# Performance work log

Hardware: AMD Instinct MI355X
Metric: run time of the kernel (lower is better)

The kernel has to match this reference:

```python
import jax, jax.numpy as jnp
import numpy as np

B, H, W, D, K = 64, 32, 32, 512, 64
EPS = 1e-12


def setup_inputs() -> dict:
    key = jax.random.key(0)
    k1, k2, k3 = jax.random.split(key, 3)
    inputs = jax.random.normal(k1, (B, H, W, D), dtype=jnp.float32)
    # 1x1 conv kernel (no bias) -> equivalent to a [D, K] matmul per pixel
    w = jax.random.normal(k2, (D, K), dtype=jnp.float32) * 0.02
    # cluster centers, stored in the original as (1,1,1,D,K); we keep [D, K]
    C = jax.random.normal(k3, (D, K), dtype=jnp.float32) * 0.02
    return {"inputs": inputs, "w": w, "C": C}


def _l2norm(v, axis=-1):
    return v / jnp.sqrt(jnp.sum(v * v, axis=axis, keepdims=True) + EPS)


def reference(inputs, w, C):
    # soft-assignment: 1x1 conv + softmax over clusters
    s = jnp.einsum('bhwd,dk->bhwk', inputs, w)          # [B,H,W,K]
    a = jax.nn.softmax(s, axis=-1)
    b, h, ww, d = inputs.shape
    k = w.shape[1]
    a2 = a.reshape(b, h * ww, k)                         # [B,N,K]
    x2 = inputs.reshape(b, h * ww, d)                    # [B,N,D]
    # VLAD reformulation: sum_n a[n,k]*(x[n,d] + C[d,k])
    #  = (a^T x)[k,d] + (sum_n a[n,k]) * C[d,k]
    # avoids materializing the [B,H,W,D,K] broadcast of the original
    vkd = jnp.einsum('bnk,bnd->bkd', a2, x2)             # [B,K,D]
    vkd = vkd + a2.sum(axis=1)[:, :, None] * C.T[None]   # [B,K,D]
    # intra-normalization over D (matches transpose->normalize in original)
    vkd = _l2norm(vkd, axis=-1)
    # transpose back to [B,D,K], flatten, global L2 normalize
    v = jnp.transpose(vkd, (0, 2, 1)).reshape(b, d * k)
    v = _l2norm(v, axis=-1)
    return v
```

## Files before the change

kernel.cpp:

```cpp
#include <hip/hip_runtime.h>

#define EPS 1e-12f
typedef __attribute__((ext_vector_type(8))) short short8;
typedef __attribute__((ext_vector_type(4))) float f32x4;

#define MFMA(a, b, c) __builtin_amdgcn_mfma_f32_16x16x32_bf16(a, b, c, 0, 0, 0)

__device__ __forceinline__ unsigned rne16(unsigned u) {
  return u + 0x7FFFu + ((u >> 16) & 1u);
}
__device__ __forceinline__ void split_pair(float f0, float f1,
                                           unsigned& hp, unsigned& lp) {
  unsigned u0 = __float_as_uint(f0), u1 = __float_as_uint(f1);
  unsigned r0 = rne16(u0), r1 = rne16(u1);
  float h0 = __uint_as_float(r0 & 0xFFFF0000u);
  float h1 = __uint_as_float(r1 & 0xFFFF0000u);
  hp = (r0 >> 16) | (r1 & 0xFFFF0000u);
  unsigned v0 = rne16(__float_as_uint(f0 - h0));
  unsigned v1 = rne16(__float_as_uint(f1 - h1));
  lp = (v0 >> 16) | (v1 & 0xFFFF0000u);
}
__device__ __forceinline__ void split8(float4 a, float4 b, short8& h, short8& l) {
  union { unsigned u[4]; short8 s; } H, L;
  split_pair(a.x, a.y, H.u[0], L.u[0]);
  split_pair(a.z, a.w, H.u[1], L.u[1]);
  split_pair(b.x, b.y, H.u[2], L.u[2]);
  split_pair(b.z, b.w, H.u[3], L.u[3]);
  h = H.s; l = L.s;
}
__device__ __forceinline__ void split8f(const float* f, short8& h, short8& l) {
  union { unsigned u[4]; short8 s; } H, L;
  split_pair(f[0], f[1], H.u[0], L.u[0]);
  split_pair(f[2], f[3], H.u[1], L.u[1]);
  split_pair(f[4], f[5], H.u[2], L.u[2]);
  split_pair(f[6], f[7], H.u[3], L.u[3]);
  h = H.s; l = L.s;
}

extern "C" __global__ __launch_bounds__(256) void netvlad_prep(
    const float* __restrict__ w, unsigned short* __restrict__ wTh,
    unsigned short* __restrict__ wTl)
{
  int tg = blockIdx.x * 256 + threadIdx.x;
  int k = tg >> 9, d = tg & 511;
  float f = w[d * 64 + k];
  unsigned u = __float_as_uint(f);
  unsigned rh = rne16(u);
  float hf = __uint_as_float(rh & 0xFFFF0000u);
  unsigned rl = rne16(__float_as_uint(f - hf));
  wTh[tg] = (unsigned short)(rh >> 16);
  wTl[tg] = (unsigned short)(rl >> 16);
}

extern "C" __global__ __launch_bounds__(256) void netvlad_assign(
    const float* __restrict__ x, const unsigned short* __restrict__ wTh,
    const unsigned short* __restrict__ wTl, unsigned short* __restrict__ aTh,
    unsigned short* __restrict__ aTl, float* __restrict__ asum)
{
  __shared__ unsigned short ath[64 * 136];
  __shared__ unsigned short atl[64 * 136];
  __shared__ float asp[4 * 64];

  const int t = threadIdx.x;
  const int lane = t & 63, wv = t >> 6;
  const int lo4 = lane & 15, hi4 = lane >> 4;
  const int b = blockIdx.x >> 3;
  const int nblk = (blockIdx.x & 7) << 7;

  f32x4 acc[2][4] = {};

  const float* xp0 =
      x + (size_t)((blockIdx.x << 7) + (wv << 5) + lo4) * 512 + (hi4 << 3);

  for (int d0 = 0; d0 < 512; d0 += 32) {
    short8 xh[2], xl[2];
#pragma unroll
    for (int pt = 0; pt < 2; ++pt) {
      const float* p = xp0 + (size_t)pt * (16 * 512) + d0;
      float4 v0 = *(const float4*)p;
      float4 v1 = *(const float4*)(p + 4);
      split8(v0, v1, xh[pt], xl[pt]);
    }
#pragma unroll
    for (int nt = 0; nt < 4; ++nt) {
      const size_t wo = (size_t)((nt << 4) + lo4) * 512 + d0 + (hi4 << 3);
      short8 wh = *(const short8*)(wTh + wo);
      short8 wl = *(const short8*)(wTl + wo);
#pragma unroll
      for (int pt = 0; pt < 2; ++pt) {
        acc[pt][nt] = MFMA(xh[pt], wh, acc[pt][nt]);
        acc[pt][nt] = MFMA(xl[pt], wh, acc[pt][nt]);
        acc[pt][nt] = MFMA(xh[pt], wl, acc[pt][nt]);
      }
    }
  }

  float asum_p[4] = {0.f, 0.f, 0.f, 0.f};
#pragma unroll
  for (int pt = 0; pt < 2; ++pt) {
#pragma unroll
    for (int r = 0; r < 4; ++r) {
      float s0 = acc[pt][0][r], s1 = acc[pt][1][r];
      float s2 = acc[pt][2][r], s3 = acc[pt][3][r];
      float m = fmaxf(fmaxf(s0, s1), fmaxf(s2, s3));
      m = fmaxf(m, __shfl_xor(m, 1));
      m = fmaxf(m, __shfl_xor(m, 2));
      m = fmaxf(m, __shfl_xor(m, 4));
      m = fmaxf(m, __shfl_xor(m, 8));
      float e0 = __expf(s0 - m), e1 = __expf(s1 - m);
      float e2 = __expf(s2 - m), e3 = __expf(s3 - m);
      float s = e0 + e1 + e2 + e3;
      s += __shfl_xor(s, 1);
      s += __shfl_xor(s, 2);
      s += __shfl_xor(s, 4);
      s += __shfl_xor(s, 8);
      float inv = 1.0f / s;
      e0 *= inv; e1 *= inv; e2 *= inv; e3 *= inv;
      asum_p[0] += e0; asum_p[1] += e1; asum_p[2] += e2; asum_p[3] += e3;
      acc[pt][0][r] = e0; acc[pt][1][r] = e1;
      acc[pt][2][r] = e2; acc[pt][3][r] = e3;
    }
  }
#pragma unroll
  for (int pt = 0; pt < 2; ++pt)
#pragma unroll
    for (int nt = 0; nt < 4; ++nt)
#pragma unroll
      for (int r = 0; r < 4; ++r) {
        float a = acc[pt][nt][r];
        unsigned u = __float_as_uint(a);
        unsigned rh = rne16(u);
        float hf = __uint_as_float(rh & 0xFFFF0000u);
        unsigned rl = rne16(__float_as_uint(a - hf));
        int idx = ((nt << 4) + lo4) * 136 + (wv << 5) + (pt << 4) + (hi4 << 2) + r;
        ath[idx] = (unsigned short)(rh >> 16);
        atl[idx] = (unsigned short)(rl >> 16);
      }
#pragma unroll
  for (int nt = 0; nt < 4; ++nt) {
    float v = asum_p[nt];
    v += __shfl_xor(v, 16);
    v += __shfl_xor(v, 32);
    if (lane < 16) asp[(wv << 6) + (nt << 4) + lane] = v;
  }
  __syncthreads();
  if (t < 64) {
    float s = asp[t] + asp[64 + t] + asp[128 + t] + asp[192 + t];
    atomicAdd(&asum[(b << 6) + t], s);
  }
  {
    const int k = t >> 2, px0 = (t & 3) << 5;
    const size_t go = ((size_t)((b << 6) + k) << 10) + nblk + px0;
#pragma unroll
    for (int c = 0; c < 4; ++c) {
      *(short8*)(aTh + go + (c << 3)) = *(short8*)&ath[k * 136 + px0 + (c << 3)];
      *(short8*)(aTl + go + (c << 3)) = *(short8*)&atl[k * 136 + px0 + (c << 3)];
    }
  }
}

extern "C" __global__ __launch_bounds__(256) void netvlad_vlad(
    const float* __restrict__ x, const unsigned short* __restrict__ aTh,
    const unsigned short* __restrict__ aTl, float* __restrict__ vkd)
{
  __shared__ float xt[64 * 68];
  const int t = threadIdx.x;
  const int lane = t & 63, wv = t >> 6;
  const int lo4 = lane & 15, hi4 = lane >> 4;
  const int b = blockIdx.x >> 3;
  const int ds = (blockIdx.x & 7) << 6;
  const int srow = t >> 2, scol = (t & 3) << 4;
  const float* xs = x + ((size_t)(b << 10)) * 512 + ds;

  f32x4 acc[4] = {};

  for (int n0 = 0; n0 < 1024; n0 += 64) {
    __syncthreads();
    {
      const float* p = xs + (size_t)(n0 + srow) * 512 + scol;
      float4 v0 = ((const float4*)p)[0];
      float4 v1 = ((const float4*)p)[1];
      float4 v2 = ((const float4*)p)[2];
      float4 v3 = ((const float4*)p)[3];
      float* dst = &xt[srow * 68 + scol];
      ((float4*)dst)[0] = v0;
      ((float4*)dst)[1] = v1;
      ((float4*)dst)[2] = v2;
      ((float4*)dst)[3] = v3;
    }
    __syncthreads();
#pragma unroll
    for (int nf = 0; nf < 2; ++nf) {
      float f[8];
#pragma unroll
      for (int j = 0; j < 8; ++j)
        f[j] = xt[((nf << 5) + (hi4 << 3) + j) * 68 + (wv << 4) + lo4];
      short8 bh, bl;
      split8f(f, bh, bl);
#pragma unroll
      for (int kt = 0; kt < 4; ++kt) {
        const size_t ao = ((size_t)((b << 6) + (kt << 4) + lo4) << 10)
                        + n0 + (nf << 5) + (hi4 << 3);
        short8 ah = *(const short8*)(aTh + ao);
        short8 al = *(const short8*)(aTl + ao);
        acc[kt] = MFMA(ah, bh, acc[kt]);
        acc[kt] = MFMA(ah, bl, acc[kt]);
        acc[kt] = MFMA(al, bh, acc[kt]);
      }
    }
  }
#pragma unroll
  for (int kt = 0; kt < 4; ++kt) {
    float* vb = vkd + (((size_t)(b << 9) + ds + (wv << 4) + lo4) << 6)
              + (kt << 4) + (hi4 << 2);
    *(float4*)vb = make_float4(acc[kt][0], acc[kt][1], acc[kt][2], acc[kt][3]);
  }
}

extern "C" __global__ __launch_bounds__(256) void netvlad_fin1(
    const float* __restrict__ vkd, const float* __restrict__ Cm,
    const float* __restrict__ asum, float* __restrict__ out,
    float* __restrict__ r_buf)
{
  __shared__ float rp[4 * 64];
  const int t = threadIdx.x;
  const int k = t & 63;
  const int dg = t >> 6;
  const int b = blockIdx.x >> 2;
  const int dq = blockIdx.x & 3;
  const float asv = asum[b * 64 + k];
  const int dbase = dq * 128 + dg * 32;
  const float* p0 = vkd + (size_t)b * 512 * 64;
  float* ob = out + (size_t)b * 512 * 64;
  float racc = 0.f;
  for (int dd = 0; dd < 32; ++dd) {
    size_t off = (size_t)(dbase + dd) * 64 + k;
    float v = p0[off] + asv * Cm[off];
    ob[off] = v;
    racc = fmaf(v, v, racc);
  }
  rp[dg * 64 + k] = racc;
  __syncthreads();
  if (t < 64) {
    float r = rp[t] + rp[64 + t] + rp[128 + t] + rp[192 + t];
    atomicAdd(&r_buf[b * 64 + t], r);
  }
}

extern "C" __global__ __launch_bounds__(64) void netvlad_fin2(
    const float* __restrict__ r_buf, float* __restrict__ scale_buf)
{
  const int b = blockIdx.x;
  const int k = threadIdx.x;
  float r = r_buf[b * 64 + k];
  float g = r / (r + EPS);
  g += __shfl_xor(g, 1);
  g += __shfl_xor(g, 2);
  g += __shfl_xor(g, 4);
  g += __shfl_xor(g, 8);
  g += __shfl_xor(g, 16);
  g += __shfl_xor(g, 32);
  scale_buf[b * 64 + k] = 1.0f / (sqrtf(r + EPS) * sqrtf(g + EPS));
}

extern "C" __global__ __launch_bounds__(256) void netvlad_fin3(
    float* __restrict__ out, const float* __restrict__ scale_buf)
{
  __shared__ float sc[64];
  const int t = threadIdx.x;
  const int b = blockIdx.x >> 3;
  if (t < 64) sc[t] = scale_buf[b * 64 + t];
  __syncthreads();
  float4* o4 = (float4*)out;
#pragma unroll
  for (int c = 0; c < 4; ++c) {
    int idx = blockIdx.x * 1024 + c * 256 + t;
    float4 v = o4[idx];
    int k4 = (idx & 15) * 4;
    v.x *= sc[k4]; v.y *= sc[k4 + 1]; v.z *= sc[k4 + 2]; v.w *= sc[k4 + 3];
    o4[idx] = v;
  }
}

extern "C" void kernel_launch(void* const* d_in, const int* in_sizes, int n_in,
                              void* d_out, int out_size, void* d_ws,
                              size_t ws_size, hipStream_t stream)
{
  const float* x  = (const float*)d_in[0];
  const float* w  = (const float*)d_in[1];
  const float* Cm = (const float*)d_in[2];
  float* out = (float*)d_out;

  unsigned short* aTh = (unsigned short*)d_ws;
  unsigned short* aTl = aTh + 4194304;
  float* vkd = (float*)(aTl + 4194304);
  unsigned short* wTh = (unsigned short*)(vkd + 2097152);
  unsigned short* wTl = wTh + 32768;
  float* asum = (float*)(wTl + 32768);
  float* r_buf = asum + 4096;
  float* scale_buf = r_buf + 4096;

  hipMemsetAsync(asum, 0, 2 * 4096 * sizeof(float), stream);

  netvlad_prep  <<<128, 256, 0, stream>>>(w, wTh, wTl);
  netvlad_assign<<<512, 256, 0, stream>>>(x, wTh, wTl, aTh, aTl, asum);
  netvlad_vlad  <<<512, 256, 0, stream>>>(x, aTh, aTl, vkd);
  netvlad_fin1  <<<256, 256, 0, stream>>>(vkd, Cm, asum, out, r_buf);
  netvlad_fin2  <<< 64,  64, 0, stream>>>(r_buf, scale_buf);
  netvlad_fin3  <<<512, 256, 0, stream>>>(out, scale_buf);
}
```

Baseline: 306.5 us.

## Double grid sizes, prefetch x, pre-split x in LDS, fuse scale kernel

The assign kernel now handles 64 pixels per block across 1024 blocks, with a one-step register prefetch of x. The vlad kernel handles 32 d-columns per block across 1024 blocks. It converts x to bf16 hi/lo once when staging into double-buffered LDS, and reads the a-matrix once per wave instead of per k-tile. fin1 is vectorised to float4 over 1024 blocks, and fin2 is folded into fin3 to remove one launch. The aim is more parallelism and fewer redundant conversions, at the cost of more global reads of x and aT across the extra blocks.

Result: faster. 294.6 us (-3.9%).

```diff
diff --git a/kernel.cpp b/kernel.cpp
--- a/kernel.cpp
+++ b/kernel.cpp
@@ -8,6 +8,15 @@
 
 __device__ __forceinline__ unsigned rne16(unsigned u) {
   return u + 0x7FFFu + ((u >> 16) & 1u);
+}
+__device__ __forceinline__ void split2(float f, unsigned short& h,
+                                       unsigned short& l) {
+  unsigned u = __float_as_uint(f);
+  unsigned rh = rne16(u);
+  float hf = __uint_as_float(rh & 0xFFFF0000u);
+  unsigned rl = rne16(__float_as_uint(f - hf));
+  h = (unsigned short)(rh >> 16);
+  l = (unsigned short)(rl >> 16);
 }
 __device__ __forceinline__ void split_pair(float f0, float f1,
                                            unsigned& hp, unsigned& lp) {
@@ -28,14 +37,6 @@
   split_pair(b.z, b.w, H.u[3], L.u[3]);
   h = H.s; l = L.s;
 }
-__device__ __forceinline__ void split8f(const float* f, short8& h, short8& l) {
-  union { unsigned u[4]; short8 s; } H, L;
-  split_pair(f[0], f[1], H.u[0], L.u[0]);
-  split_pair(f[2], f[3], H.u[1], L.u[1]);
-  split_pair(f[4], f[5], H.u[2], L.u[2]);
-  split_pair(f[6], f[7], H.u[3], L.u[3]);
-  h = H.s; l = L.s;
-}
 
 extern "C" __global__ __launch_bounds__(256) void netvlad_prep(
     const float* __restrict__ w, unsigned short* __restrict__ wTh,
@@ -43,13 +44,10 @@
 {
   int tg = blockIdx.x * 256 + threadIdx.x;
   int k = tg >> 9, d = tg & 511;
-  float f = w[d * 64 + k];
-  unsigned u = __float_as_uint(f);
-  unsigned rh = rne16(u);
-  float hf = __uint_as_float(rh & 0xFFFF0000u);
-  unsigned rl = rne16(__float_as_uint(f - hf));
-  wTh[tg] = (unsigned short)(rh >> 16);
-  wTl[tg] = (unsigned short)(rl >> 16);
+  unsigned short h, l;
+  split2(w[d * 64 + k], h, l);
+  wTh[tg] = h;
+  wTl[tg] = l;
 }
 
 extern "C" __global__ __launch_bounds__(256) void netvlad_assign(
@@ -57,85 +55,72 @@
     const unsigned short* __restrict__ wTl, unsigned short* __restrict__ aTh,
     unsigned short* __restrict__ aTl, float* __restrict__ asum)
 {
-  __shared__ unsigned short ath[64 * 136];
-  __shared__ unsigned short atl[64 * 136];
+  __shared__ unsigned short ath[64 * 72];
+  __shared__ unsigned short atl[64 * 72];
   __shared__ float asp[4 * 64];
 
   const int t = threadIdx.x;
   const int lane = t & 63, wv = t >> 6;
   const int lo4 = lane & 15, hi4 = lane >> 4;
-  const int b = blockIdx.x >> 3;
-  const int nblk = (blockIdx.x & 7) << 7;
-
-  f32x4 acc[2][4] = {};
-
-  const float* xp0 =
-      x + (size_t)((blockIdx.x << 7) + (wv << 5) + lo4) * 512 + (hi4 << 3);
-
+  const int b = blockIdx.x >> 4;
+  const int nblk = (blockIdx.x & 15) << 6;
+
+  f32x4 acc[4] = {};
+
+  const float* xp =
+      x + ((size_t)(blockIdx.x << 6) + (wv << 4) + lo4) * 512 + (hi4 << 3);
+
+  float4 c0 = *(const float4*)xp;
+  float4 c1 = *(const float4*)(xp + 4);
   for (int d0 = 0; d0 < 512; d0 += 32) {
-    short8 xh[2], xl[2];
-#pragma unroll
-    for (int pt = 0; pt < 2; ++pt) {
-      const float* p = xp0 + (size_t)pt * (16 * 512) + d0;
-      float4 v0 = *(const float4*)p;
-      float4 v1 = *(const float4*)(p + 4);
-      split8(v0, v1, xh[pt], xl[pt]);
-    }
+    const float* np = xp + ((d0 < 480) ? d0 + 32 : 0);
+    float4 n0v = *(const float4*)np;
+    float4 n1v = *(const float4*)(np + 4);
+    short8 xh, xl;
+    split8(c0, c1, xh, xl);
 #pragma unroll
     for (int nt = 0; nt < 4; ++nt) {
       const size_t wo = (size_t)((nt << 4) + lo4) * 512 + d0 + (hi4 << 3);
       short8 wh = *(const short8*)(wTh + wo);
       short8 wl = *(const short8*)(wTl + wo);
-#pragma unroll
-      for (int pt = 0; pt < 2; ++pt) {
-        acc[pt][nt] = MFMA(xh[pt], wh, acc[pt][nt]);
-        acc[pt][nt] = MFMA(xl[pt], wh, acc[pt][nt]);
-        acc[pt][nt] = MFMA(xh[pt], wl, acc[pt][nt]);
-      }
-    }
+      acc[nt] = MFMA(xh, wh, acc[nt]);
+      acc[nt] = MFMA(xl, wh, acc[nt]);
+      acc[nt] = MFMA(xh, wl, acc[nt]);
+    }
+    c0 = n0v; c1 = n1v;
   }
 
   float asum_p[4] = {0.f, 0.f, 0.f, 0.f};
 #pragma unroll
-  for (int pt = 0; pt < 2; ++pt) {
+  for (int r = 0; r < 4; ++r) {
+    float s0 = acc[0][r], s1 = acc[1][r], s2 = acc[2][r], s3 = acc[3][r];
+    float m = fmaxf(fmaxf(s0, s1), fmaxf(s2, s3));
+    m = fmaxf(m, __shfl_xor(m, 1));
+    m = fmaxf(m, __shfl_xor(m, 2));
+    m = fmaxf(m, __shfl_xor(m, 4));
+    m = fmaxf(m, __shfl_xor(m, 8));
+    float e0 = __expf(s0 - m), e1 = __expf(s1 - m);
+    float e2 = __expf(s2 - m), e3 = __expf(s3 - m);
+    float s = e0 + e1 + e2 + e3;
+    s += __shfl_xor(s, 1);
+    s += __shfl_xor(s, 2);
+    s += __shfl_xor(s, 4);
+    s += __shfl_xor(s, 8);
+    float inv = 1.0f / s;
+    e0 *= inv; e1 *= inv; e2 *= inv; e3 *= inv;
+    asum_p[0] += e0; asum_p[1] += e1; asum_p[2] += e2; asum_p[3] += e3;
+    acc[0][r] = e0; acc[1][r] = e1; acc[2][r] = e2; acc[3][r] = e3;
+  }
+#pragma unroll
+  for (int nt = 0; nt < 4; ++nt)
 #pragma unroll
     for (int r = 0; r < 4; ++r) {
-      float s0 = acc[pt][0][r], s1 = acc[pt][1][r];
-      float s2 = acc[pt][2][r], s3 = acc[pt][3][r];
-      float m = fmaxf(fmaxf(s0, s1), fmaxf(s2, s3));
-      m = fmaxf(m, __shfl_xor(m, 1));
-      m = fmaxf(m, __shfl_xor(m, 2));
-      m = fmaxf(m, __shfl_xor(m, 4));
-      m = fmaxf(m, __shfl_xor(m, 8));
-      float e0 = __expf(s0 - m), e1 = __expf(s1 - m);
-      float e2 = __expf(s2 - m), e3 = __expf(s3 - m);
-      float s = e0 + e1 + e2 + e3;
-      s += __shfl_xor(s, 1);
-      s += __shfl_xor(s, 2);
-      s += __shfl_xor(s, 4);
-      s += __shfl_xor(s, 8);
-      float inv = 1.0f / s;
-      e0 *= inv; e1 *= inv; e2 *= inv; e3 *= inv;
-      asum_p[0] += e0; asum_p[1] += e1; asum_p[2] += e2; asum_p[3] += e3;
-      acc[pt][0][r] = e0; acc[pt][1][r] = e1;
-      acc[pt][2][r] = e2; acc[pt][3][r] = e3;
-    }
-  }
-#pragma unroll
-  for (int pt = 0; pt < 2; ++pt)
-#pragma unroll
-    for (int nt = 0; nt < 4; ++nt)
-#pragma unroll
-      for (int r = 0; r < 4; ++r) {
-        float a = acc[pt][nt][r];
-        unsigned u = __float_as_uint(a);
-        unsigned rh = rne16(u);
-        float hf = __uint_as_float(rh & 0xFFFF0000u);
-        unsigned rl = rne16(__float_as_uint(a - hf));
-        int idx = ((nt << 4) + lo4) * 136 + (wv << 5) + (pt << 4) + (hi4 << 2) + r;
-        ath[idx] = (unsigned short)(rh >> 16);
-        atl[idx] = (unsigned short)(rl >> 16);
-      }
+      unsigned short h, l;
+      split2(acc[nt][r], h, l);
+      int idx = ((nt << 4) + lo4) * 72 + (wv << 4) + (hi4 << 2) + r;
+      ath[idx] = h;
+      atl[idx] = l;
+    }
 #pragma unroll
   for (int nt = 0; nt < 4; ++nt) {
     float v = asum_p[nt];
@@ -149,13 +134,12 @@
     atomicAdd(&asum[(b << 6) + t], s);
   }
   {
-    const int k = t >> 2, px0 = (t & 3) << 5;
+    const int k = t >> 2, px0 = (t & 3) << 4;
     const size_t go = ((size_t)((b << 6) + k) << 10) + nblk + px0;
-#pragma unroll
-    for (int c = 0; c < 4; ++c) {
-      *(short8*)(aTh + go + (c << 3)) = *(short8*)&ath[k * 136 + px0 + (c << 3)];
-      *(short8*)(aTl + go + (c << 3)) = *(short8*)&atl[k * 136 + px0 + (c << 3)];
-    }
+    *(short8*)(aTh + go)     = *(short8*)&ath[k * 72 + px0];
+    *(short8*)(aTh + go + 8) = *(short8*)&ath[k * 72 + px0 + 8];
+    *(short8*)(aTl + go)     = *(short8*)&atl[k * 72 + px0];
+    *(short8*)(aTl + go + 8) = *(short8*)&atl[k * 72 + px0 + 8];
   }
 }
 
@@ -163,57 +147,62 @@
     const float* __restrict__ x, const unsigned short* __restrict__ aTh,
     const unsigned short* __restrict__ aTl, float* __restrict__ vkd)
 {
-  __shared__ float xt[64 * 68];
+  __shared__ unsigned short xth[2][32 * 72];
+  __shared__ unsigned short xtl[2][32 * 72];
   const int t = threadIdx.x;
   const int lane = t & 63, wv = t >> 6;
   const int lo4 = lane & 15, hi4 = lane >> 4;
-  const int b = blockIdx.x >> 3;
-  const int ds = (blockIdx.x & 7) << 6;
-  const int srow = t >> 2, scol = (t & 3) << 4;
-  const float* xs = x + ((size_t)(b << 10)) * 512 + ds;
-
-  f32x4 acc[4] = {};
-
-  for (int n0 = 0; n0 < 1024; n0 += 64) {
+  const int b = blockIdx.x >> 4;
+  const int ds = (blockIdx.x & 15) << 5;
+  const int tn = t & 63;
+  const int tdc = (t >> 6) << 3;
+  const float* xsb = x + ((size_t)(b << 10)) * 512 + ds + tdc;
+
+  f32x4 acc[2] = {};
+
+  float4 r0 = *(const float4*)(xsb + (size_t)tn * 512);
+  float4 r1 = *(const float4*)(xsb + (size_t)tn * 512 + 4);
+
+  for (int it = 0; it < 16; ++it) {
+    const int n0 = it << 6;
+    unsigned short* th = xth[it & 1];
+    unsigned short* tl = xtl[it & 1];
+    float f[8] = {r0.x, r0.y, r0.z, r0.w, r1.x, r1.y, r1.z, r1.w};
+#pragma unroll
+    for (int j = 0; j < 8; ++j) {
+      unsigned short h, l;
+      split2(f[j], h, l);
+      th[(tdc + j) * 72 + tn] = h;
+      tl[(tdc + j) * 72 + tn] = l;
+    }
     __syncthreads();
-    {
-      const float* p = xs + (size_t)(n0 + srow) * 512 + scol;
-      float4 v0 = ((const float4*)p)[0];
-      float4 v1 = ((const float4*)p)[1];
-      float4 v2 = ((const float4*)p)[2];
-      float4 v3 = ((const float4*)p)[3];
-      float* dst = &xt[srow * 68 + scol];
-      ((float4*)dst)[0] = v0;
-      ((float4*)dst)[1] = v1;
-      ((float4*)dst)[2] = v2;
-      ((float4*)dst)[3] = v3;
-    }
-    __syncthreads();
+    if (it < 15) {
+      const float* p = xsb + (size_t)(n0 + 64 + tn) * 512;
+      r0 = *(const float4*)p;
+      r1 = *(const float4*)(p + 4);
+    }
 #pragma unroll
     for (int nf = 0; nf < 2; ++nf) {
-      float f[8];
-#pragma unroll
-      for (int j = 0; j < 8; ++j)
-        f[j] = xt[((nf << 5) + (hi4 << 3) + j) * 68 + (wv << 4) + lo4];
-      short8 bh, bl;
-      split8f(f, bh, bl);
-#pragma unroll
-      for (int kt = 0; kt < 4; ++kt) {
-        const size_t ao = ((size_t)((b << 6) + (kt << 4) + lo4) << 10)
-                        + n0 + (nf << 5) + (hi4 << 3);
-        short8 ah = *(const short8*)(aTh + ao);
-        short8 al = *(const short8*)(aTl + ao);
-        acc[kt] = MFMA(ah, bh, acc[kt]);
-        acc[kt] = MFMA(ah, bl, acc[kt]);
-        acc[kt] = MFMA(al, bh, acc[kt]);
+      const size_t ao = ((size_t)((b << 6) + (wv << 4) + lo4) << 10)
+                      + n0 + (nf << 5) + (hi4 << 3);
+      short8 ah = *(const short8*)(aTh + ao);
+      short8 al = *(const short8*)(aTl + ao);
+#pragma unroll
+      for (int dt = 0; dt < 2; ++dt) {
+        const int xo = ((dt << 4) + lo4) * 72 + (nf << 5) + (hi4 << 3);
+        short8 bh = *(short8*)&th[xo];
+        short8 bl = *(short8*)&tl[xo];
+        acc[dt] = MFMA(ah, bh, acc[dt]);
+        acc[dt] = MFMA(ah, bl, acc[dt]);
+        acc[dt] = MFMA(al, bh, acc[dt]);
       }
     }
   }
 #pragma unroll
-  for (int kt = 0; kt < 4; ++kt) {
-    float* vb = vkd + (((size_t)(b << 9) + ds + (wv << 4) + lo4) << 6)
-              + (kt << 4) + (hi4 << 2);
-    *(float4*)vb = make_float4(acc[kt][0], acc[kt][1], acc[kt][2], acc[kt][3]);
+  for (int dt = 0; dt < 2; ++dt) {
+    float* vb = vkd + (((size_t)(b << 9) + ds + (dt << 4) + lo4) << 6)
+              + (wv << 4) + (hi4 << 2);
+    *(float4*)vb = make_float4(acc[dt][0], acc[dt][1], acc[dt][2], acc[dt][3]);
   }
 }
 
@@ -222,54 +211,53 @@
     const float* __restrict__ asum, float* __restrict__ out,
     float* __restrict__ r_buf)
 {
-  __shared__ float rp[4 * 64];
-  const int t = threadIdx.x;
-  const int k = t & 63;
-  const int dg = t >> 6;
-  const int b = blockIdx.x >> 2;
-  const int dq = blockIdx.x & 3;
-  const float asv = asum[b * 64 + k];
-  const int dbase = dq * 128 + dg * 32;
-  const float* p0 = vkd + (size_t)b * 512 * 64;
-  float* ob = out + (size_t)b * 512 * 64;
-  float racc = 0.f;
-  for (int dd = 0; dd < 32; ++dd) {
-    size_t off = (size_t)(dbase + dd) * 64 + k;
-    float v = p0[off] + asv * Cm[off];
-    ob[off] = v;
-    racc = fmaf(v, v, racc);
-  }
-  rp[dg * 64 + k] = racc;
+  __shared__ float rp[16 * 64];
+  const int t = threadIdx.x;
+  const int b = blockIdx.x >> 4;
+  const int ds = (blockIdx.x & 15) << 5;
+  const int k4 = (t & 15) << 2;
+  const int dg = t >> 4;
+  float4 asv = *(const float4*)(asum + (b << 6) + k4);
+  float4 racc = {0.f, 0.f, 0.f, 0.f};
+#pragma unroll
+  for (int j = 0; j < 2; ++j) {
+    int d = ds + dg * 2 + j;
+    size_t off = (((size_t)(b << 9) + d) << 6) + k4;
+    float4 v = *(const float4*)(vkd + off);
+    float4 c = *(const float4*)(Cm + ((size_t)d << 6) + k4);
+    v.x += asv.x * c.x; v.y += asv.y * c.y;
+    v.z += asv.z * c.z; v.w += asv.w * c.w;
+    *(float4*)(out + off) = v;
+    racc.x = fmaf(v.x, v.x, racc.x); racc.y = fmaf(v.y, v.y, racc.y);
+    racc.z = fmaf(v.z, v.z, racc.z); racc.w = fmaf(v.w, v.w, racc.w);
+  }
+  *(float4*)&rp[dg * 64 + k4] = racc;
   __syncthreads();
   if (t < 64) {
-    float r = rp[t] + rp[64 + t] + rp[128 + t] + rp[192 + t];
-    atomicAdd(&r_buf[b * 64 + t], r);
-  }
-}
-
-extern "C" __global__ __launch_bounds__(64) void netvlad_fin2(
-    const float* __restrict__ r_buf, float* __restrict__ scale_buf)
-{
-  const int b = blockIdx.x;
-  const int k = threadIdx.x;
-  float r = r_buf[b * 64 + k];
-  float g = r / (r + EPS);
-  g += __shfl_xor(g, 1);
-  g += __shfl_xor(g, 2);
-  g += __shfl_xor(g, 4);
-  g += __shfl_xor(g, 8);
-  g += __shfl_xor(g, 16);
-  g += __shfl_xor(g, 32);
-  scale_buf[b * 64 + k] = 1.0f / (sqrtf(r + EPS) * sqrtf(g + EPS));
+    float r = 0.f;
+#pragma unroll
+    for (int g = 0; g < 16; ++g) r += rp[g * 64 + t];
+    atomicAdd(&r_buf[(b << 6) + t], r);
+  }
 }
 
 extern "C" __global__ __launch_bounds__(256) void netvlad_fin3(
-    float* __restrict__ out, const float* __restrict__ scale_buf)
+    float* __restrict__ out, const float* __restrict__ r_buf)
 {
   __shared__ float sc[64];
   const int t = threadIdx.x;
   const int b = blockIdx.x >> 3;
-  if (t < 64) sc[t] = scale_buf[b * 64 + t];
+  if (t < 64) {
+    float r = r_buf[(b << 6) + t];
+    float g = r / (r + EPS);
+    g += __shfl_xor(g, 1);
+    g += __shfl_xor(g, 2);
+    g += __shfl_xor(g, 4);
+    g += __shfl_xor(g, 8);
+    g += __shfl_xor(g, 16);
+    g += __shfl_xor(g, 32);
+    sc[t] = 1.0f / (sqrtf(r + EPS) * sqrtf(g + EPS));
+  }
   __syncthreads();
   float4* o4 = (float4*)out;
 #pragma unroll
@@ -298,14 +286,12 @@
   unsigned short* wTl = wTh + 32768;
   float* asum = (float*)(wTl + 32768);
   float* r_buf = asum + 4096;
-  float* scale_buf = r_buf + 4096;
 
   hipMemsetAsync(asum, 0, 2 * 4096 * sizeof(float), stream);
 
-  netvlad_prep  <<<128, 256, 0, stream>>>(w, wTh, wTl);
-  netvlad_assign<<<512, 256, 0, stream>>>(x, wTh, wTl, aTh, aTl, asum);
-  netvlad_vlad  <<<512, 256, 0, stream>>>(x, aTh, aTl, vkd);
-  netvlad_fin1  <<<256, 256, 0, stream>>>(vkd, Cm, asum, out, r_buf);
-  netvlad_fin2  <<< 64,  64, 0, stream>>>(r_buf, scale_buf);
-  netvlad_fin3  <<<512, 256, 0, stream>>>(out, scale_buf);
-}
+  netvlad_prep  <<< 128, 256, 0, stream>>>(w, wTh, wTl);
+  netvlad_assign<<<1024, 256, 0, stream>>>(x, wTh, wTl, aTh, aTl, asum);
+  netvlad_vlad  <<<1024, 256, 0, stream>>>(x, aTh, aTl, vkd);
+  netvlad_fin1  <<<1024, 256, 0, stream>>>(vkd, Cm, asum, out, r_buf);
+  netvlad_fin3  <<< 512, 256, 0, stream>>>(out, r_buf);
+}
```
